# Kernel tuning notes

Hardware: AMD Instinct MI355X
Metric: run time of the kernel (lower is better)

The kernel has to match this reference:

```python
import jax, jax.numpy as jnp
import numpy as np

B, D_IN, H, OUT = 65536, 3072, 100, 10
CUTOFF = 0.5


def setup_inputs() -> dict:
    key = jax.random.key(0)
    ks = jax.random.split(key, 7)
    x = jax.random.normal(ks[0], (B, D_IN), jnp.float32)
    # Kaiming-ish scaling so activations stay sane through 15 relu layers
    w_in = jax.random.normal(ks[1], (D_IN, H), jnp.float32) * np.float32(1.0 / np.sqrt(D_IN))
    b_in = jax.random.normal(ks[2], (H,), jnp.float32) * np.float32(0.01)
    w_hid = jax.random.normal(ks[3], (14, H, H), jnp.float32) * np.float32(1.0 / np.sqrt(H))
    b_hid = jax.random.normal(ks[4], (14, H), jnp.float32) * np.float32(0.01)
    w_out = jax.random.normal(ks[5], (3, H, OUT), jnp.float32) * np.float32(1.0 / np.sqrt(H))
    b_out = jax.random.normal(ks[6], (3, OUT), jnp.float32) * np.float32(0.01)
    return {"x": x, "w_in": w_in, "b_in": b_in, "w_hid": w_hid, "b_hid": b_hid, "w_out": w_out, "b_out": b_out}


def reference(x, w_in, b_in, w_hid, b_hid, w_out, b_out):
    # Stage 0 (net0): first layer D_IN->H then 4 hidden layers H->H, all relu
    h = jax.nn.relu(x @ w_in + b_in)
    for i in range(0, 4):
        h = jax.nn.relu(h @ w_hid[i] + b_hid[i])
    out0 = h @ w_out[0] + b_out[0]                     # [B, 10]
    conf0 = jnp.max(out0, axis=1) > CUTOFF             # cutoff_mask

    # Stage 1 (net1): 5 hidden layers H->H on net0's hidden features
    for i in range(4, 9):
        h = jax.nn.relu(h @ w_hid[i] + b_hid[i])
    out1 = h @ w_out[1] + b_out[1]
    conf1 = jnp.max(out1, axis=1) > CUTOFF

    # Stage 2 (net2): 5 hidden layers H->H, output registered unconditionally
    for i in range(9, 14):
        h = jax.nn.relu(h @ w_hid[i] + b_hid[i])
    out2 = h @ w_out[2] + b_out[2]

    # Filter/reordered_output: each sample takes the output of the first stage
    # at which it was confident (early-exit cascade, dense-masked equivalent).
    final = jnp.where(conf0[:, None], out0, jnp.where(conf1[:, None], out1, out2))
    return final
```

## Files before the change

kernel.cpp:

```cpp
#include <hip/hip_runtime.h>


typedef __fp16 h2   __attribute__((ext_vector_type(2)));
typedef __fp16 h8v  __attribute__((ext_vector_type(8)));
typedef float  f4v  __attribute__((ext_vector_type(4)));
typedef float  f16v __attribute__((ext_vector_type(16)));

#define CHUNK 16384

static constexpr unsigned OFF_W1  = 0;
static constexpr unsigned OFF_WH  = 96u * CHUNK;
static constexpr unsigned OFF_WO  = OFF_WH + 56u * CHUNK;
static constexpr unsigned OFF_BIN = OFF_WO + 3u * CHUNK;
static constexpr unsigned OFF_H1  = OFF_BIN + 512;

__device__ __forceinline__ unsigned bc2(h2 v) { return __builtin_bit_cast(unsigned, v); }

__device__ __forceinline__ f4v ntld4(const float* p) {
  return __builtin_nontemporal_load((const f4v*)p);
}

__device__ __forceinline__ void lds_cp16(const char* g, char* l) {
  __builtin_amdgcn_global_load_lds(
      (const __attribute__((address_space(1))) void*)g,
      (__attribute__((address_space(3))) void*)l, 16, 0, 0);
}

__device__ __forceinline__ void stage2(const char* g, char* l, int tid) {
  lds_cp16(g + tid * 16, l + tid * 16);
  lds_cp16(g + 8192 + tid * 16, l + 8192 + tid * 16);
}

__device__ __forceinline__ void cvt8(f4v a, f4v b, h8v& hi, h8v& lo) {
  h2 h0 = __builtin_amdgcn_cvt_pkrtz(a[0], a[1]);
  h2 h1 = __builtin_amdgcn_cvt_pkrtz(a[2], a[3]);
  h2 h2_ = __builtin_amdgcn_cvt_pkrtz(b[0], b[1]);
  h2 h3 = __builtin_amdgcn_cvt_pkrtz(b[2], b[3]);
  h2 l0 = __builtin_amdgcn_cvt_pkrtz(a[0] - (float)h0[0], a[1] - (float)h0[1]);
  h2 l1 = __builtin_amdgcn_cvt_pkrtz(a[2] - (float)h1[0], a[3] - (float)h1[1]);
  h2 l2 = __builtin_amdgcn_cvt_pkrtz(b[0] - (float)h2_[0], b[1] - (float)h2_[1]);
  h2 l3 = __builtin_amdgcn_cvt_pkrtz(b[2] - (float)h3[0], b[3] - (float)h3[1]);
  hi = h8v{h0[0], h0[1], h1[0], h1[1], h2_[0], h2_[1], h3[0], h3[1]};
  lo = h8v{l0[0], l0[1], l1[0], l1[1], l2[0], l2[1], l3[0], l3[1]};
}

__device__ __forceinline__ void split4s(f4v v, uint2& hi, uint2& lo) {
  h2 a = __builtin_amdgcn_cvt_pkrtz(v[0], v[1]);
  h2 b = __builtin_amdgcn_cvt_pkrtz(v[2], v[3]);
  h2 c = __builtin_amdgcn_cvt_pkrtz(v[0] - (float)a[0], v[1] - (float)a[1]);
  h2 d = __builtin_amdgcn_cvt_pkrtz(v[2] - (float)b[0], v[3] - (float)b[1]);
  hi = make_uint2(bc2(a), bc2(b));
  lo = make_uint2(bc2(c), bc2(d));
}

__device__ __forceinline__ void split8w(const float* f, uint4& hi, uint4& lo) {
  h2 h0 = __builtin_amdgcn_cvt_pkrtz(f[0], f[1]);
  h2 h1 = __builtin_amdgcn_cvt_pkrtz(f[2], f[3]);
  h2 h2_ = __builtin_amdgcn_cvt_pkrtz(f[4], f[5]);
  h2 h3 = __builtin_amdgcn_cvt_pkrtz(f[6], f[7]);
  h2 l0 = __builtin_amdgcn_cvt_pkrtz(f[0] - (float)h0[0], f[1] - (float)h0[1]);
  h2 l1 = __builtin_amdgcn_cvt_pkrtz(f[2] - (float)h1[0], f[3] - (float)h1[1]);
  h2 l2 = __builtin_amdgcn_cvt_pkrtz(f[4] - (float)h2_[0], f[5] - (float)h2_[1]);
  h2 l3 = __builtin_amdgcn_cvt_pkrtz(f[6] - (float)h3[0], f[7] - (float)h3[1]);
  hi = make_uint4(bc2(h0), bc2(h1), bc2(h2_), bc2(h3));
  lo = make_uint4(bc2(l0), bc2(l1), bc2(l2), bc2(l3));
}

__device__ __forceinline__ unsigned item_off(int it) {
  if (it >= 58) return OFF_WO + 2u * CHUNK;
  if (it == 16) return OFF_WO;
  if (it == 37) return OFF_WO + CHUNK;
  int j = it - (it > 16 ? 1 : 0) - (it > 37 ? 1 : 0);
  return OFF_WH + (unsigned)j * CHUNK;
}

__global__ __launch_bounds__(256) void prep_k(
    const float* __restrict__ w_in, const float* __restrict__ b_in,
    const float* __restrict__ w_hid, const float* __restrict__ b_hid,
    const float* __restrict__ w_out, const float* __restrict__ b_out,
    char* __restrict__ ws) {
  int idx = blockIdx.x * 256 + threadIdx.x;
  int lane = idx & 63;
  int grp = idx >> 6;
  float f[8];
  uint4 hi, lo;
  if (grp < 768) {
    int mf = grp & 7, c = grp >> 3;
    int feat = mf * 16 + (lane & 15);
    int g = lane >> 4;
    int kb = c * 32 + g * 4;
#pragma unroll
    for (int e = 0; e < 8; ++e) {
      int k = kb + (e < 4 ? e : 12 + e);
      f[e] = (feat < 100) ? w_in[(size_t)k * 100 + feat] : 0.f;
    }
    split8w(f, hi, lo);
    char* dst = ws + OFF_W1 + (size_t)c * CHUNK + (size_t)mf * 2048 + lane * 16;
    *(uint4*)dst = hi;
    *(uint4*)(dst + 1024) = lo;
    return;
  }
  grp -= 768;
  if (grp < 448) {
    int j = grp & 1, ft = (grp >> 1) & 3, ch = grp >> 3;
    int L = ch >> 2, s = ch & 3;
    int feat = ft * 32 + (lane & 31);
    int k0 = s * 32 + j * 16 + (lane >> 5) * 8;
#pragma unroll
    for (int e = 0; e < 8; ++e) {
      int k = k0 + e;
      float v;
      if (k < 100 && feat < 100)  v = w_hid[(size_t)L * 10000 + k * 100 + feat];
      else if (k == 127)          v = (feat < 100) ? b_hid[L * 100 + feat]
                                                   : (feat == 127 ? 1.f : 0.f);
      else                        v = 0.f;
      f[e] = v;
    }
    split8w(f, hi, lo);
    char* dst = ws + OFF_WH + (size_t)ch * CHUNK + (size_t)((ft * 2 + j) * 2) * 1024 + lane * 16;
    *(uint4*)dst = hi;
    *(uint4*)(dst + 1024) = lo;
    return;
  }
  grp -= 448;
  if (grp < 24) {
    int kb = grp & 7, st = grp >> 3;
    int cls = lane & 31;
    int k0 = kb * 16 + (lane >> 5) * 8;
#pragma unroll
    for (int e = 0; e < 8; ++e) {
      int k = k0 + e;
      float v;
      if (cls < 10 && k < 100) v = w_out[(size_t)st * 1000 + k * 10 + cls];
      else if (k == 127)       v = (cls < 10) ? b_out[st * 10 + cls] : -60000.f;
      else                     v = 0.f;
      f[e] = v;
    }
    split8w(f, hi, lo);
    char* dst = ws + OFF_WO + (size_t)st * CHUNK + (size_t)(kb * 2) * 1024 + lane * 16;
    *(uint4*)dst = hi;
    *(uint4*)(dst + 1024) = lo;
    return;
  }
  grp -= 24;
  if (grp < 2) {
    int i = grp * 64 + lane;
    ((float*)(ws + OFF_BIN))[i] = (i < 100) ? b_in[i] : (i == 127 ? 1.f : 0.f);
  }
}

#define P1_SMEM (3 * CHUNK)

__global__ __launch_bounds__(512, 4) void p1_k(const float* __restrict__ x,
                                               char* __restrict__ ws) {
  extern __shared__ __align__(16) char sm[];
  const int tid = threadIdx.x;
  const int lane = tid & 63, wid = tid >> 6;
  const int l15 = lane & 15, g = lane >> 4;
  const int tile = blockIdx.x;
  const char* w1g = ws + OFF_W1;
  const float* xr = x + (size_t)(tile * 128 + wid * 16 + l15) * 3072;

  f4v xP[2], xQ[2], xR[2];
  stage2(w1g, sm, tid);
  __builtin_amdgcn_sched_barrier(0);
  xP[0] = ntld4(xr + g * 4);      xP[1] = ntld4(xr + 16 + g * 4);
  __builtin_amdgcn_sched_barrier(0);
  stage2(w1g + CHUNK, sm + CHUNK, tid);
  __builtin_amdgcn_sched_barrier(0);
  xQ[0] = ntld4(xr + 32 + g * 4); xQ[1] = ntld4(xr + 48 + g * 4);
  __builtin_amdgcn_sched_barrier(0);
  xR[0] = ntld4(xr + 64 + g * 4); xR[1] = ntld4(xr + 80 + g * 4);
  __builtin_amdgcn_sched_barrier(0);

  f4v acc[8] = {};
  const int abase = lane * 16;

  auto step = [&](int s, f4v (&xa)[2]) {
    if (s <= 93)      asm volatile("s_waitcnt vmcnt(6)" ::: "memory");
    else if (s == 94) asm volatile("s_waitcnt vmcnt(4)" ::: "memory");
    else              asm volatile("s_waitcnt vmcnt(0)" ::: "memory");
    __builtin_amdgcn_s_barrier();
    asm volatile("" ::: "memory");

    h8v bhi, blo;
    cvt8(xa[0], xa[1], bhi, blo);
    if (s + 2 < 96) stage2(w1g + (size_t)(s + 2) * CHUNK, sm + ((s + 2) % 3) * CHUNK, tid);
    __builtin_amdgcn_sched_barrier(0);
    if (s + 3 < 96) {
      const int o = (s + 3) * 32 + g * 4;
      xa[0] = ntld4(xr + o); xa[1] = ntld4(xr + o + 16);
    }
    __builtin_amdgcn_sched_barrier(0);

    const char* ab = sm + (s % 3) * CHUNK + abase;
#pragma unroll
    for (int mf = 0; mf < 8; ++mf) {
      h8v ahi = *(const h8v*)(ab + mf * 2048);
      h8v alo = *(const h8v*)(ab + mf * 2048 + 1024);
      acc[mf] = __builtin_amdgcn_mfma_f32_16x16x32_f16(ahi, bhi, acc[mf], 0, 0, 0);
      acc[mf] = __builtin_amdgcn_mfma_f32_16x16x32_f16(ahi, blo, acc[mf], 0, 0, 0);
      acc[mf] = __builtin_amdgcn_mfma_f32_16x16x32_f16(alo, bhi, acc[mf], 0, 0, 0);
    }
  };

#pragma unroll 1
  for (int s3 = 0; s3 < 96; s3 += 3) {
    step(s3, xP);
    step(s3 + 1, xQ);
    step(s3 + 2, xR);
  }

  const float* bp = (const float*)(ws + OFF_BIN);
  const int rt = wid >> 1;
  const int l31 = (wid & 1) * 16 + l15;
  char* hb = ws + OFF_H1 + (size_t)tile * 65536;
#pragma unroll
  for (int mf = 0; mf < 8; ++mf) {
    f4v bi = *(const f4v*)(bp + mf * 16 + g * 4);
    f4v v = acc[mf] + bi;
    v[0] = fmaxf(v[0], 0.f); v[1] = fmaxf(v[1], 0.f);
    v[2] = fmaxf(v[2], 0.f); v[3] = fmaxf(v[3], 0.f);
    uint2 hi, lo;
    split4s(v, hi, lo);
    char* dst = hb + (size_t)(rt * 8 + mf) * 2048 + (g >> 1) * 512 + l31 * 16 + (g & 1) * 8;
    *(uint2*)dst = hi;
    *(uint2*)(dst + 1024) = lo;
  }
}

#define P2_SMEM (65536 + 3 * CHUNK)

__global__ __launch_bounds__(512, 2) void p2_k(char* __restrict__ ws,
                                               float* __restrict__ out) {
  extern __shared__ __align__(16) char sm[];
  char* hsm = sm;
  char* wsm = sm + 65536;
  const int tid = threadIdx.x;
  const int lane = tid & 63, wid = tid >> 6;
  const int mr = wid & 1, rt = wid >> 1;
  const int l31 = lane & 31, gg = lane >> 5;
  const int tile = blockIdx.x;

  {
    const char* hg = ws + OFF_H1 + (size_t)tile * 65536;
#pragma unroll
    for (int i = 0; i < 8; ++i)
      lds_cp16(hg + i * 8192 + tid * 16, hsm + i * 8192 + tid * 16);
    __builtin_amdgcn_sched_barrier(0);
    stage2(ws + item_off(0), wsm, tid);
    stage2(ws + item_off(1), wsm + CHUNK, tid);
  }

  const f16v z16 = {};
  f16v a0 = {}, a1 = {};
  float s0[6], s1[6], s2[6];
  bool c0 = false, c1 = false;

  auto ring_top = [&](int i) {
    asm volatile("s_waitcnt vmcnt(2)" ::: "memory");
    __builtin_amdgcn_s_barrier();
    asm volatile("" ::: "memory");
    stage2(ws + item_off(i + 2), wsm + ((i + 2) % 3) * CHUNK, tid);
  };

  auto hidden = [&](int base) {
#pragma unroll
    for (int ss = 0; ss < 4; ++ss) {
      ring_top(base + ss);
      const char* wb = wsm + ((base + ss) % 3) * CHUNK + lane * 16;
      const char* hbp = hsm + rt * 16384 + ss * 4096 + lane * 16;
      h8v bh0 = *(const h8v*)(hbp);
      h8v bl0 = *(const h8v*)(hbp + 1024);
      h8v bh1 = *(const h8v*)(hbp + 2048);
      h8v bl1 = *(const h8v*)(hbp + 3072);
      const char* ab0 = wb + (mr * 2) * 4096;
      const char* ab1 = ab0 + 4096;
      h8v ah, al;
      ah = *(const h8v*)(ab0);        al = *(const h8v*)(ab0 + 1024);
      a0 = __builtin_amdgcn_mfma_f32_32x32x16_f16(ah, bh0, a0, 0, 0, 0);
      a0 = __builtin_amdgcn_mfma_f32_32x32x16_f16(ah, bl0, a0, 0, 0, 0);
      a0 = __builtin_amdgcn_mfma_f32_32x32x16_f16(al, bh0, a0, 0, 0, 0);
      ah = *(const h8v*)(ab0 + 2048); al = *(const h8v*)(ab0 + 3072);
      a0 = __builtin_amdgcn_mfma_f32_32x32x16_f16(ah, bh1, a0, 0, 0, 0);
      a0 = __builtin_amdgcn_mfma_f32_32x32x16_f16(ah, bl1, a0, 0, 0, 0);
      a0 = __builtin_amdgcn_mfma_f32_32x32x16_f16(al, bh1, a0, 0, 0, 0);
      ah = *(const h8v*)(ab1);        al = *(const h8v*)(ab1 + 1024);
      a1 = __builtin_amdgcn_mfma_f32_32x32x16_f16(ah, bh0, a1, 0, 0, 0);
      a1 = __builtin_amdgcn_mfma_f32_32x32x16_f16(ah, bl0, a1, 0, 0, 0);
      a1 = __builtin_amdgcn_mfma_f32_32x32x16_f16(al, bh0, a1, 0, 0, 0);
      ah = *(const h8v*)(ab1 + 2048); al = *(const h8v*)(ab1 + 3072);
      a1 = __builtin_amdgcn_mfma_f32_32x32x16_f16(ah, bh1, a1, 0, 0, 0);
      a1 = __builtin_amdgcn_mfma_f32_32x32x16_f16(ah, bl1, a1, 0, 0, 0);
      a1 = __builtin_amdgcn_mfma_f32_32x32x16_f16(al, bh1, a1, 0, 0, 0);
    }
    __builtin_amdgcn_s_barrier();
    asm volatile("" ::: "memory");
#pragma unroll
    for (int fi = 0; fi < 2; ++fi) {
      const int ftb = mr * 2 + fi;
#pragma unroll
      for (int q = 0; q < 4; ++q) {
        f4v v = fi ? f4v{a1[4 * q], a1[4 * q + 1], a1[4 * q + 2], a1[4 * q + 3]}
                   : f4v{a0[4 * q], a0[4 * q + 1], a0[4 * q + 2], a0[4 * q + 3]};
        v[0] = fmaxf(v[0], 0.f); v[1] = fmaxf(v[1], 0.f);
        v[2] = fmaxf(v[2], 0.f); v[3] = fmaxf(v[3], 0.f);
        uint2 hi, lo;
        split4s(v, hi, lo);
        const int kblk = ftb * 2 + (q >> 1);
        char* dst = hsm + (size_t)((rt * 8 + kblk) * 2) * 1024 + ((q & 1) * 32 + l31) * 16 + gg * 8;
        *(uint2*)dst = hi;
        *(uint2*)(dst + 1024) = lo;
      }
    }
    asm volatile("s_waitcnt lgkmcnt(0)" ::: "memory");
    __builtin_amdgcn_s_barrier();
    asm volatile("" ::: "memory");
    a0 = z16;
    a1 = z16;
  };

  auto wstage = [&](int i, float (&sv)[6], bool* cb) {
    ring_top(i);
    const char* wb = wsm + (i % 3) * CHUNK + lane * 16;
    if (mr == 0) {
      f16v oa = {};
#pragma unroll
      for (int kb = 0; kb < 8; ++kb) {
        h8v ah = *(const h8v*)(wb + kb * 2048);
        h8v al = *(const h8v*)(wb + kb * 2048 + 1024);
        const char* hbp = hsm + rt * 16384 + kb * 2048 + lane * 16;
        h8v bh = *(const h8v*)(hbp);
        h8v bl = *(const h8v*)(hbp + 1024);
        oa = __builtin_amdgcn_mfma_f32_32x32x16_f16(ah, bh, oa, 0, 0, 0);
        oa = __builtin_amdgcn_mfma_f32_32x32x16_f16(ah, bl, oa, 0, 0, 0);
        oa = __builtin_amdgcn_mfma_f32_32x32x16_f16(al, bh, oa, 0, 0, 0);
      }
      float m = oa[0];
#pragma unroll
      for (int r = 1; r < 16; ++r) m = fmaxf(m, oa[r]);
      m = fmaxf(m, __shfl_xor(m, 32, 64));
      if (cb) *cb = (m > 0.5f);
      sv[0] = oa[0]; sv[1] = oa[1]; sv[2] = oa[2];
      sv[3] = oa[3]; sv[4] = oa[4]; sv[5] = oa[5];
    }
  };

  hidden(0); hidden(4); hidden(8); hidden(12);
  wstage(16, s0, &c0);
  hidden(17); hidden(21); hidden(25); hidden(29); hidden(33);
  wstage(37, s1, &c1);
  hidden(38); hidden(42); hidden(46); hidden(50); hidden(54);
  wstage(58, s2, nullptr);

  if (mr == 0) {
    float r[6];
#pragma unroll
    for (int j = 0; j < 6; ++j) r[j] = c0 ? s0[j] : (c1 ? s1[j] : s2[j]);
    float* dp = out + (size_t)(tile * 128 + rt * 32 + l31) * 10;
    if (gg == 0) {
      *(float2*)(dp)     = make_float2(r[0], r[1]);
      *(float2*)(dp + 2) = make_float2(r[2], r[3]);
      *(float2*)(dp + 8) = make_float2(r[4], r[5]);
    } else {
      *(float2*)(dp + 4) = make_float2(r[0], r[1]);
      *(float2*)(dp + 6) = make_float2(r[2], r[3]);
    }
  }
}

extern "C" void kernel_launch(void* const* d_in, const int* in_sizes, int n_in,
                              void* d_out, int out_size, void* d_ws, size_t ws_size,
                              hipStream_t stream) {
  (void)in_sizes; (void)n_in; (void)out_size; (void)ws_size;
  const float* x     = (const float*)d_in[0];
  const float* w_in  = (const float*)d_in[1];
  const float* b_in  = (const float*)d_in[2];
  const float* w_hid = (const float*)d_in[3];
  const float* b_hid = (const float*)d_in[4];
  const float* w_out = (const float*)d_in[5];
  const float* b_out = (const float*)d_in[6];
  float* out = (float*)d_out;
  char* ws = (char*)d_ws;

  (void)hipFuncSetAttribute((const void*)p1_k,
                            hipFuncAttributeMaxDynamicSharedMemorySize, P1_SMEM);
  (void)hipFuncSetAttribute((const void*)p2_k,
                            hipFuncAttributeMaxDynamicSharedMemorySize, P2_SMEM);

  prep_k<<<311, 256, 0, stream>>>(w_in, b_in, w_hid, b_hid, w_out, b_out, ws);
  p1_k<<<512, 512, P1_SMEM, stream>>>(x, ws);
  p2_k<<<512, 512, P2_SMEM, stream>>>(ws, out);
}
```

Before: 328.2 us.

## Stage x through LDS with coalesced loads and deepen p2 weight ring

The first-layer kernel now loads x with row-contiguous coalesced 16-byte loads. It converts each value to a hi/lo fp16 pair and writes it into a swizzled, double-buffered LDS tile instead of converting directly in registers. It processes two weight chunks per step with a 128KB shared-memory footprint, which lowers occupancy from 4 to 2 blocks per CU. The hidden-layer kernel grows its weight ring from 3 to 4 slots so prefetch runs one item further ahead. The extra LDS round trip and barrier per step add overhead that has to be paid back by better global-memory coalescing.

```diff
diff --git a/kernel.cpp b/kernel.cpp
--- a/kernel.cpp
+++ b/kernel.cpp
@@ -29,19 +29,6 @@
 __device__ __forceinline__ void stage2(const char* g, char* l, int tid) {
   lds_cp16(g + tid * 16, l + tid * 16);
   lds_cp16(g + 8192 + tid * 16, l + 8192 + tid * 16);
-}
-
-__device__ __forceinline__ void cvt8(f4v a, f4v b, h8v& hi, h8v& lo) {
-  h2 h0 = __builtin_amdgcn_cvt_pkrtz(a[0], a[1]);
-  h2 h1 = __builtin_amdgcn_cvt_pkrtz(a[2], a[3]);
-  h2 h2_ = __builtin_amdgcn_cvt_pkrtz(b[0], b[1]);
-  h2 h3 = __builtin_amdgcn_cvt_pkrtz(b[2], b[3]);
-  h2 l0 = __builtin_amdgcn_cvt_pkrtz(a[0] - (float)h0[0], a[1] - (float)h0[1]);
-  h2 l1 = __builtin_amdgcn_cvt_pkrtz(a[2] - (float)h1[0], a[3] - (float)h1[1]);
-  h2 l2 = __builtin_amdgcn_cvt_pkrtz(b[0] - (float)h2_[0], b[1] - (float)h2_[1]);
-  h2 l3 = __builtin_amdgcn_cvt_pkrtz(b[2] - (float)h3[0], b[3] - (float)h3[1]);
-  hi = h8v{h0[0], h0[1], h1[0], h1[1], h2_[0], h2_[1], h3[0], h3[1]};
-  lo = h8v{l0[0], l0[1], l1[0], l1[1], l2[0], l2[1], l3[0], l3[1]};
 }
 
 __device__ __forceinline__ void split4s(f4v v, uint2& hi, uint2& lo) {
@@ -149,68 +136,119 @@
   }
 }
 
-#define P1_SMEM (3 * CHUNK)
-
-__global__ __launch_bounds__(512, 4) void p1_k(const float* __restrict__ x,
+#define P1_SMEM 131072
+
+__global__ __launch_bounds__(512, 2) void p1_k(const float* __restrict__ x,
                                                char* __restrict__ ws) {
   extern __shared__ __align__(16) char sm[];
+  char* xbuf = sm;
+  char* wbuf = sm + 65536;
+
   const int tid = threadIdx.x;
   const int lane = tid & 63, wid = tid >> 6;
-  const int l15 = lane & 15, g = lane >> 4;
+  const int g = lane >> 4;
+  const int j = lane & 15;
   const int tile = blockIdx.x;
   const char* w1g = ws + OFF_W1;
-  const float* xr = x + (size_t)(tile * 128 + wid * 16 + l15) * 3072;
-
-  f4v xP[2], xQ[2], xR[2];
-  stage2(w1g, sm, tid);
+
+  const float* xr[4];
+#pragma unroll
+  for (int q = 0; q < 4; ++q)
+    xr[q] = x + (size_t)(tile * 128 + wid * 16 + q * 4 + g) * 3072 + j * 4;
+
+  int xwo[4];
+  {
+    const int kc = j >> 3, jj = j & 7, gw = jj & 3, half = jj >> 2;
+#pragma unroll
+    for (int q = 0; q < 4; ++q) {
+      const int r = q * 4 + g;
+      const int fl = gw * 16 + r;
+      const int phi = fl ^ (gw << 2);
+      xwo[q] = wid * 4096 + kc * 2048 + phi * 16 + half * 8;
+    }
+  }
+  const int xro = wid * 4096 + (lane ^ ((lane >> 4) << 2)) * 16;
+
+  auto stW = [&](int s1, int b) {
+    const char* gsrc = w1g + (size_t)(2 * s1) * CHUNK;
+    char* dst = wbuf + b * 32768;
+#pragma unroll
+    for (int i = 0; i < 4; ++i)
+      lds_cp16(gsrc + i * 8192 + tid * 16, dst + i * 8192 + tid * 16);
+  };
+  auto ldx = [&](int s1, f4v (&xa)[4]) {
+    const int o = s1 * 64;
+#pragma unroll
+    for (int q = 0; q < 4; ++q) xa[q] = ntld4(xr[q] + o);
+  };
+  auto wrx = [&](int s1, f4v (&xa)[4]) {
+    char* base = xbuf + (s1 & 1) * 32768;
+#pragma unroll
+    for (int q = 0; q < 4; ++q) {
+      uint2 hi, lo;
+      split4s(xa[q], hi, lo);
+      char* d = base + xwo[q];
+      *(uint2*)d = hi;
+      *(uint2*)(d + 1024) = lo;
+    }
+  };
+
+  f4v xP[4], xQ[4];
+  ldx(0, xP);
   __builtin_amdgcn_sched_barrier(0);
-  xP[0] = ntld4(xr + g * 4);      xP[1] = ntld4(xr + 16 + g * 4);
+  stW(0, 0);
   __builtin_amdgcn_sched_barrier(0);
-  stage2(w1g + CHUNK, sm + CHUNK, tid);
+  ldx(1, xQ);
   __builtin_amdgcn_sched_barrier(0);
-  xQ[0] = ntld4(xr + 32 + g * 4); xQ[1] = ntld4(xr + 48 + g * 4);
+  asm volatile("s_waitcnt vmcnt(8)" ::: "memory");
+  wrx(0, xP);
   __builtin_amdgcn_sched_barrier(0);
-  xR[0] = ntld4(xr + 64 + g * 4); xR[1] = ntld4(xr + 80 + g * 4);
+  ldx(2, xP);
   __builtin_amdgcn_sched_barrier(0);
+  asm volatile("s_waitcnt lgkmcnt(0)" ::: "memory");
 
   f4v acc[8] = {};
-  const int abase = lane * 16;
-
-  auto step = [&](int s, f4v (&xa)[2]) {
-    if (s <= 93)      asm volatile("s_waitcnt vmcnt(6)" ::: "memory");
-    else if (s == 94) asm volatile("s_waitcnt vmcnt(4)" ::: "memory");
-    else              asm volatile("s_waitcnt vmcnt(0)" ::: "memory");
+
+  auto step = [&](int s, f4v (&xa)[4]) {
+    if (s >= 46) asm volatile("s_waitcnt vmcnt(0)" ::: "memory");
+    else         asm volatile("s_waitcnt vmcnt(4)" ::: "memory");
     __builtin_amdgcn_s_barrier();
     asm volatile("" ::: "memory");
 
-    h8v bhi, blo;
-    cvt8(xa[0], xa[1], bhi, blo);
-    if (s + 2 < 96) stage2(w1g + (size_t)(s + 2) * CHUNK, sm + ((s + 2) % 3) * CHUNK, tid);
+    if (s < 47) wrx(s + 1, xa);
     __builtin_amdgcn_sched_barrier(0);
-    if (s + 3 < 96) {
-      const int o = (s + 3) * 32 + g * 4;
-      xa[0] = ntld4(xr + o); xa[1] = ntld4(xr + o + 16);
-    }
+    if (s + 1 < 48) stW(s + 1, (s + 1) & 1);
     __builtin_amdgcn_sched_barrier(0);
-
-    const char* ab = sm + (s % 3) * CHUNK + abase;
-#pragma unroll
-    for (int mf = 0; mf < 8; ++mf) {
-      h8v ahi = *(const h8v*)(ab + mf * 2048);
-      h8v alo = *(const h8v*)(ab + mf * 2048 + 1024);
-      acc[mf] = __builtin_amdgcn_mfma_f32_16x16x32_f16(ahi, bhi, acc[mf], 0, 0, 0);
-      acc[mf] = __builtin_amdgcn_mfma_f32_16x16x32_f16(ahi, blo, acc[mf], 0, 0, 0);
-      acc[mf] = __builtin_amdgcn_mfma_f32_16x16x32_f16(alo, bhi, acc[mf], 0, 0, 0);
+    if (s + 3 < 48) ldx(s + 3, xa);
+    __builtin_amdgcn_sched_barrier(0);
+    asm volatile("s_waitcnt lgkmcnt(0)" ::: "memory");
+    __builtin_amdgcn_s_barrier();
+    asm volatile("" ::: "memory");
+
+    const char* xb = xbuf + (s & 1) * 32768 + xro;
+    const char* ab = wbuf + (s & 1) * 32768 + lane * 16;
+#pragma unroll
+    for (int kc = 0; kc < 2; ++kc) {
+      h8v bh = *(const h8v*)(xb + kc * 2048);
+      h8v bl = *(const h8v*)(xb + kc * 2048 + 1024);
+#pragma unroll
+      for (int mf = 0; mf < 8; ++mf) {
+        h8v ahi = *(const h8v*)(ab + kc * 16384 + mf * 2048);
+        h8v alo = *(const h8v*)(ab + kc * 16384 + mf * 2048 + 1024);
+        acc[mf] = __builtin_amdgcn_mfma_f32_16x16x32_f16(ahi, bh, acc[mf], 0, 0, 0);
+        acc[mf] = __builtin_amdgcn_mfma_f32_16x16x32_f16(ahi, bl, acc[mf], 0, 0, 0);
+        acc[mf] = __builtin_amdgcn_mfma_f32_16x16x32_f16(alo, bh, acc[mf], 0, 0, 0);
+      }
     }
   };
 
 #pragma unroll 1
-  for (int s3 = 0; s3 < 96; s3 += 3) {
-    step(s3, xP);
-    step(s3 + 1, xQ);
-    step(s3 + 2, xR);
-  }
-
+  for (int s2 = 0; s2 < 48; s2 += 2) {
+    step(s2, xQ);
+    step(s2 + 1, xP);
+  }
+
+  const int l15 = lane & 15;
   const float* bp = (const float*)(ws + OFF_BIN);
   const int rt = wid >> 1;
   const int l31 = (wid & 1) * 16 + l15;
@@ -229,7 +267,7 @@
   }
 }
 
-#define P2_SMEM (65536 + 3 * CHUNK)
+#define P2_SMEM (65536 + 4 * CHUNK)
 
 __global__ __launch_bounds__(512, 2) void p2_k(char* __restrict__ ws,
                                                float* __restrict__ out) {
@@ -250,6 +288,7 @@
     __builtin_amdgcn_sched_barrier(0);
     stage2(ws + item_off(0), wsm, tid);
     stage2(ws + item_off(1), wsm + CHUNK, tid);
+    stage2(ws + item_off(2), wsm + 2 * CHUNK, tid);
   }
 
   const f16v z16 = {};
@@ -258,17 +297,17 @@
   bool c0 = false, c1 = false;
 
   auto ring_top = [&](int i) {
-    asm volatile("s_waitcnt vmcnt(2)" ::: "memory");
+    asm volatile("s_waitcnt vmcnt(4)" ::: "memory");
     __builtin_amdgcn_s_barrier();
     asm volatile("" ::: "memory");
-    stage2(ws + item_off(i + 2), wsm + ((i + 2) % 3) * CHUNK, tid);
+    stage2(ws + item_off(i + 3), wsm + ((i + 3) & 3) * CHUNK, tid);
   };
 
   auto hidden = [&](int base) {
 #pragma unroll
     for (int ss = 0; ss < 4; ++ss) {
       ring_top(base + ss);
-      const char* wb = wsm + ((base + ss) % 3) * CHUNK + lane * 16;
+      const char* wb = wsm + ((base + ss) & 3) * CHUNK + lane * 16;
       const char* hbp = hsm + rt * 16384 + ss * 4096 + lane * 16;
       h8v bh0 = *(const h8v*)(hbp);
       h8v bl0 = *(const h8v*)(hbp + 1024);
@@ -322,7 +361,7 @@
 
   auto wstage = [&](int i, float (&sv)[6], bool* cb) {
     ring_top(i);
-    const char* wb = wsm + (i % 3) * CHUNK + lane * 16;
+    const char* wb = wsm + (i & 3) * CHUNK + lane * 16;
     if (mr == 0) {
       f16v oa = {};
 #pragma unroll
```

Result: faster. 321.8 us (-2.0%).
